# Optimization experiments

Measured on AMD Instinct MI355X. Metric: run time of the kernel, lower is better.

Reference implementation:

```python
import jax, jax.numpy as jnp
from jax import lax
import numpy as np

BATCH = 131072
D_IN = 512
D_OUT = 512
ITERS = 10
THRES = 1e-6


def bjorck_orthonormalize(w, iters=ITERS, thres=THRES):
    """Order-1 Bjorck orthonormalization: W <- 1.5*W - 0.5*W (W^T W).

    Row-orthogonal if out<=in, column-orthogonal otherwise (operate on W^T).
    Early-stops when max|delta| <= thres, matching the module's tolerance.
    """
    transpose = w.shape[0] > w.shape[1]
    if transpose:
        w = w.T

    def cond(state):
        i, _, err = state
        return jnp.logical_and(i < iters, err > thres)

    def body(state):
        i, w, _ = state
        w_new = 1.5 * w - 0.5 * (w @ (w.T @ w))
        err = jnp.max(jnp.abs(w_new - w))
        return i + 1, w_new, err

    _, w, _ = lax.while_loop(
        cond, body, (jnp.array(0, jnp.int32), w, jnp.array(jnp.inf, w.dtype))
    )
    if transpose:
        w = w.T
    return w


def setup_inputs() -> dict:
    key = jax.random.key(0)
    k1, k2 = jax.random.split(key)
    inputs = jax.random.normal(k1, (BATCH, D_IN), dtype=jnp.float32)
    # scaled Gaussian so singular values lie in (0, sqrt(3)) -> Bjorck converges
    weight = jax.random.normal(k2, (D_OUT, D_IN), dtype=jnp.float32) * (0.5 / np.sqrt(D_IN))
    return {"inputs": inputs, "weight": weight}


def reference(inputs, weight):
    # training-mode forward with projection=True, inverse=False:
    # weight.data <- bjorck(weight.data); out = F.linear(inputs, weight)
    w_proj = bjorck_orthonormalize(weight)
    return inputs @ w_proj.T  # [batch, out_features]
```

## Files before the change

### kernel.cpp

```cpp
#include <hip/hip_runtime.h>


using bf16x8 = __attribute__((ext_vector_type(8))) short;
using f32x4  = __attribute__((ext_vector_type(4))) float;
using u16x8  = __attribute__((ext_vector_type(8))) unsigned short;

#define DI 512

__device__ __forceinline__ unsigned short f2bf(float f) {
  unsigned int u = __builtin_bit_cast(unsigned int, f);
  u += 0x7FFFu + ((u >> 16) & 1u);
  return (unsigned short)(u >> 16);
}
__device__ __forceinline__ float bf2f(unsigned short h) {
  unsigned int u = ((unsigned int)h) << 16;
  return __builtin_bit_cast(float, u);
}

__global__ void k_split(const float* __restrict__ W, float* __restrict__ Wm,
                        unsigned short* __restrict__ Wh, unsigned short* __restrict__ Wl,
                        unsigned short* __restrict__ WTh, unsigned short* __restrict__ WTl) {
  int idx = blockIdx.x * blockDim.x + threadIdx.x;
  int m = idx >> 9, i = idx & 511;
  float w = W[idx];
  Wm[idx] = w;
  unsigned short h  = f2bf(w);
  unsigned short lo = f2bf(w - bf2f(h));
  Wh[idx] = h; Wl[idx] = lo;
  WTh[i * DI + m] = h; WTl[i * DI + m] = lo;
}

__global__ __launch_bounds__(256) void k_mm2(
    const unsigned short* __restrict__ Ah, const unsigned short* __restrict__ Al,
    const unsigned short* __restrict__ Bh, const unsigned short* __restrict__ Bl,
    int mode,
    const float* __restrict__ Wm_in, float* __restrict__ Wm_out,
    unsigned short* __restrict__ Oh, unsigned short* __restrict__ Ol,
    unsigned short* __restrict__ OTh, unsigned short* __restrict__ OTl) {
  const int tid = threadIdx.x;
  const int l = tid & 63, lw = tid >> 6;
  const int wid = (blockIdx.x << 2) | lw;
  const int tile = wid >> 1, half = wid & 1;
  const int m0 = (tile >> 5) << 4, n0 = (tile & 31) << 4;
  const int kb = half << 8;
  const int lm = l & 15, lk = l >> 4;
  const int ra = (m0 + lm) * DI + kb + (lk << 3);
  const int rb = (n0 + lm) * DI + kb + (lk << 3);

  __shared__ f32x4 red[2][64];
  const int pr = lw >> 1;

  f32x4 a0{}, a1{}, a2{}, a3{}, a4{}, a5{};
#pragma unroll
  for (int k0 = 0; k0 < 256; k0 += 64) {
    bf16x8 ah0 = *(const bf16x8*)&Ah[ra + k0];
    bf16x8 al0 = *(const bf16x8*)&Al[ra + k0];
    bf16x8 bh0 = *(const bf16x8*)&Bh[rb + k0];
    bf16x8 bl0 = *(const bf16x8*)&Bl[rb + k0];
    bf16x8 ah1 = *(const bf16x8*)&Ah[ra + k0 + 32];
    bf16x8 al1 = *(const bf16x8*)&Al[ra + k0 + 32];
    bf16x8 bh1 = *(const bf16x8*)&Bh[rb + k0 + 32];
    bf16x8 bl1 = *(const bf16x8*)&Bl[rb + k0 + 32];
    a0 = __builtin_amdgcn_mfma_f32_16x16x32_bf16(ah0, bh0, a0, 0, 0, 0);
    a1 = __builtin_amdgcn_mfma_f32_16x16x32_bf16(ah0, bl0, a1, 0, 0, 0);
    a2 = __builtin_amdgcn_mfma_f32_16x16x32_bf16(al0, bh0, a2, 0, 0, 0);
    a3 = __builtin_amdgcn_mfma_f32_16x16x32_bf16(ah1, bh1, a3, 0, 0, 0);
    a4 = __builtin_amdgcn_mfma_f32_16x16x32_bf16(ah1, bl1, a4, 0, 0, 0);
    a5 = __builtin_amdgcn_mfma_f32_16x16x32_bf16(al1, bh1, a5, 0, 0, 0);
  }
  f32x4 acc = (a0 + a1) + (a2 + a3) + (a4 + a5);

  if (half) red[pr][l] = acc;
  __syncthreads();
  if (!half) {
    acc += red[pr][l];
    const int r0 = m0 + (lk << 2);
    const int cn = n0 + lm;
#pragma unroll
    for (int r = 0; r < 4; ++r) {
      const int gm = r0 + r, gn = cn;
      const float v = acc[r];
      if (mode == 0) {
        unsigned short h = f2bf(v);
        Oh[gm * DI + gn] = h;
        Ol[gm * DI + gn] = f2bf(v - bf2f(h));
      } else {
        const float wn = 1.5f * Wm_in[gm * DI + gn] - 0.5f * v;
        Wm_out[gm * DI + gn] = wn;
        unsigned short h = f2bf(wn), lo = f2bf(wn - bf2f(h));
        Oh[gm * DI + gn] = h;   Ol[gm * DI + gn] = lo;
        OTh[gn * DI + gm] = h;  OTl[gn * DI + gm] = lo;
      }
    }
  }
}

#if defined(__has_builtin)
#if __has_builtin(__builtin_amdgcn_global_load_lds)
#define HAVE_GLDS 1
#endif
#endif

#ifdef HAVE_GLDS
__device__ __forceinline__ void gl2lds16(const unsigned short* g, unsigned short* lds) {
  __builtin_amdgcn_global_load_lds(
      (const __attribute__((address_space(1))) void*)g,
      (__attribute__((address_space(3))) void*)lds, 16, 0, 0);
}
#endif

__global__ __launch_bounds__(256, 2) void k_big(
    const float* __restrict__ X, const unsigned short* __restrict__ Wp,
    float* __restrict__ out) {
  __shared__ unsigned short sA[2][2048];
  __shared__ unsigned short sB[2][16384];
  const int tid = threadIdx.x;
  const int w = tid >> 6, l = tid & 63;
  const int lm = l & 15, lk = l >> 4;
  const int ck = lk ^ ((lm >> 1) & 3);
  const int rowbase = blockIdx.x << 6;

  const int arow = tid >> 2, ac = tid & 3;
  const int alds = (arow * 4 + (ac ^ ((arow >> 1) & 3))) * 8;
  const float* xsrc = &X[(rowbase + arow) * DI + ac * 8];

  const int brow_l = l >> 2;
  const int bcs = (l & 3) ^ ((brow_l >> 1) & 3);

  f32x4 acc[4][8] = {};

  auto stage_b = [&](int kk, int bb) {
#pragma unroll
    for (int ph = 0; ph < 8; ++ph) {
      const int rowblk = ph * 64 + w * 16;
      const unsigned short* src = &Wp[(rowblk + brow_l) * DI + (kk << 5) + bcs * 8];
#ifdef HAVE_GLDS
      gl2lds16(src, &sB[bb][rowblk * 32]);
#else
      u16x8 v = *(const u16x8*)src;
      *(u16x8*)&sB[bb][rowblk * 32 + l * 8] = v;
#endif
    }
  };

  f32x4 xv0 = *(const f32x4*)xsrc;
  f32x4 xv1 = *(const f32x4*)(xsrc + 4);
  stage_b(0, 0);
  {
    u16x8 h;
    h[0] = f2bf(xv0[0]); h[1] = f2bf(xv0[1]); h[2] = f2bf(xv0[2]); h[3] = f2bf(xv0[3]);
    h[4] = f2bf(xv1[0]); h[5] = f2bf(xv1[1]); h[6] = f2bf(xv1[2]); h[7] = f2bf(xv1[3]);
    *(u16x8*)&sA[0][alds] = h;
  }
  __syncthreads();

  for (int k = 0; k < 16; ++k) {
    const int buf = k & 1;
    if (k < 15) {
      xv0 = *(const f32x4*)(xsrc + ((k + 1) << 5));
      xv1 = *(const f32x4*)(xsrc + ((k + 1) << 5) + 4);
      stage_b(k + 1, buf ^ 1);
    }
    bf16x8 a[4], b[8];
#pragma unroll
    for (int mf = 0; mf < 4; ++mf)
      a[mf] = *(const bf16x8*)&sA[buf][((mf * 16 + lm) * 4 + ck) * 8];
#pragma unroll
    for (int nf = 0; nf < 8; ++nf)
      b[nf] = *(const bf16x8*)&sB[buf][((w * 128 + nf * 16 + lm) * 4 + ck) * 8];
#pragma unroll
    for (int mf = 0; mf < 4; ++mf)
#pragma unroll
      for (int nf = 0; nf < 8; ++nf)
        acc[mf][nf] = __builtin_amdgcn_mfma_f32_16x16x32_bf16(b[nf], a[mf], acc[mf][nf], 0, 0, 0);
    if (k < 15) {
      u16x8 h;
      h[0] = f2bf(xv0[0]); h[1] = f2bf(xv0[1]); h[2] = f2bf(xv0[2]); h[3] = f2bf(xv0[3]);
      h[4] = f2bf(xv1[0]); h[5] = f2bf(xv1[1]); h[6] = f2bf(xv1[2]); h[7] = f2bf(xv1[3]);
      *(u16x8*)&sA[buf ^ 1][alds] = h;
    }
    __syncthreads();
  }

#pragma unroll
  for (int mf = 0; mf < 4; ++mf) {
    const int gm = rowbase + (mf << 4) + lm;
#pragma unroll
    for (int nf = 0; nf < 8; ++nf) {
      const int gn = (w << 7) + (nf << 4) + (lk << 2);
      *(f32x4*)&out[gm * DI + gn] = acc[mf][nf];
    }
  }
}

extern "C" void kernel_launch(void* const* d_in, const int* in_sizes, int n_in,
                              void* d_out, int out_size, void* d_ws, size_t ws_size,
                              hipStream_t stream) {
  const float* X = (const float*)d_in[0];
  const float* W = (const float*)d_in[1];
  float* out = (float*)d_out;

  char* ws = (char*)d_ws;
  size_t off = 0;
  auto carve = [&](size_t bytes) { void* p = ws + off; off += (bytes + 255) & ~(size_t)255; return p; };

  const size_t F32 = (size_t)DI * DI * 4;
  const size_t BF  = (size_t)DI * DI * 2;

  float* Wm[2];           unsigned short *Wh[2], *Wl[2], *WTh[2], *WTl[2];
  Wm[0]  = (float*)carve(F32);          Wm[1]  = (float*)carve(F32);
  Wh[0]  = (unsigned short*)carve(BF);  Wh[1]  = (unsigned short*)carve(BF);
  Wl[0]  = (unsigned short*)carve(BF);  Wl[1]  = (unsigned short*)carve(BF);
  WTh[0] = (unsigned short*)carve(BF);  WTh[1] = (unsigned short*)carve(BF);
  WTl[0] = (unsigned short*)carve(BF);  WTl[1] = (unsigned short*)carve(BF);
  unsigned short* Gh = (unsigned short*)carve(BF);
  unsigned short* Gl = (unsigned short*)carve(BF);

  k_split<<<1024, 256, 0, stream>>>(W, Wm[0], Wh[0], Wl[0], WTh[0], WTl[0]);

  int cur = 0;
  for (int it = 0; it < 10; ++it) {
    k_mm2<<<512, 256, 0, stream>>>(WTh[cur], WTl[cur], WTh[cur], WTl[cur], 0,
                                   nullptr, nullptr, Gh, Gl, nullptr, nullptr);
    const int nxt = cur ^ 1;
    k_mm2<<<512, 256, 0, stream>>>(Wh[cur], Wl[cur], Gh, Gl, 1,
                                   Wm[cur], Wm[nxt], Wh[nxt], Wl[nxt], WTh[nxt], WTl[nxt]);
    cur = nxt;
  }

  k_big<<<2048, 256, 0, stream>>>(X, Wh[cur], out);
}
```

Measured before the change: 391.2 us.

## Overlap X bf16 conversion with Bjorck iterations using extra blocks

```diff
diff --git a/kernel.cpp b/kernel.cpp
--- a/kernel.cpp
+++ b/kernel.cpp
@@ -6,6 +6,9 @@
 using u16x8  = __attribute__((ext_vector_type(8))) unsigned short;
 
 #define DI 512
+#define MFMA16(a, b, c) __builtin_amdgcn_mfma_f32_16x16x32_bf16(a, b, c, 0, 0, 0)
+#define XTOT 67108864LL
+#define XSLICE 6711296LL
 
 __device__ __forceinline__ unsigned short f2bf(float f) {
   unsigned int u = __builtin_bit_cast(unsigned int, f);
@@ -36,8 +39,25 @@
     int mode,
     const float* __restrict__ Wm_in, float* __restrict__ Wm_out,
     unsigned short* __restrict__ Oh, unsigned short* __restrict__ Ol,
-    unsigned short* __restrict__ OTh, unsigned short* __restrict__ OTl) {
+    unsigned short* __restrict__ OTh, unsigned short* __restrict__ OTl,
+    const float* __restrict__ Xsrc, unsigned short* __restrict__ Xb, int slice) {
   const int tid = threadIdx.x;
+  if (blockIdx.x >= 512) {
+    if (Xb == nullptr) return;
+    long long s0 = (long long)slice * XSLICE;
+    long long send = s0 + XSLICE; if (send > XTOT) send = XTOT;
+    for (long long i = s0 + ((long long)(blockIdx.x - 512) * 256 + tid) * 8;
+         i < send; i += 1024LL * 256 * 8) {
+      f32x4 v0 = *(const f32x4*)&Xsrc[i];
+      f32x4 v1 = *(const f32x4*)&Xsrc[i + 4];
+      u16x8 h;
+      h[0] = f2bf(v0[0]); h[1] = f2bf(v0[1]); h[2] = f2bf(v0[2]); h[3] = f2bf(v0[3]);
+      h[4] = f2bf(v1[0]); h[5] = f2bf(v1[1]); h[6] = f2bf(v1[2]); h[7] = f2bf(v1[3]);
+      *(u16x8*)&Xb[i] = h;
+    }
+    return;
+  }
+
   const int l = tid & 63, lw = tid >> 6;
   const int wid = (blockIdx.x << 2) | lw;
   const int tile = wid >> 1, half = wid & 1;
@@ -61,12 +81,12 @@
     bf16x8 al1 = *(const bf16x8*)&Al[ra + k0 + 32];
     bf16x8 bh1 = *(const bf16x8*)&Bh[rb + k0 + 32];
     bf16x8 bl1 = *(const bf16x8*)&Bl[rb + k0 + 32];
-    a0 = __builtin_amdgcn_mfma_f32_16x16x32_bf16(ah0, bh0, a0, 0, 0, 0);
-    a1 = __builtin_amdgcn_mfma_f32_16x16x32_bf16(ah0, bl0, a1, 0, 0, 0);
-    a2 = __builtin_amdgcn_mfma_f32_16x16x32_bf16(al0, bh0, a2, 0, 0, 0);
-    a3 = __builtin_amdgcn_mfma_f32_16x16x32_bf16(ah1, bh1, a3, 0, 0, 0);
-    a4 = __builtin_amdgcn_mfma_f32_16x16x32_bf16(ah1, bl1, a4, 0, 0, 0);
-    a5 = __builtin_amdgcn_mfma_f32_16x16x32_bf16(al1, bh1, a5, 0, 0, 0);
+    a0 = MFMA16(ah0, bh0, a0);
+    a1 = MFMA16(ah0, bl0, a1);
+    a2 = MFMA16(al0, bh0, a2);
+    a3 = MFMA16(ah1, bh1, a3);
+    a4 = MFMA16(ah1, bl1, a4);
+    a5 = MFMA16(al1, bh1, a5);
   }
   f32x4 acc = (a0 + a1) + (a2 + a3) + (a4 + a5);
 
@@ -109,25 +129,94 @@
 }
 #endif
 
-__global__ __launch_bounds__(256, 2) void k_big(
-    const float* __restrict__ X, const unsigned short* __restrict__ Wp,
+__global__ __launch_bounds__(256, 2) void k_big_bf(
+    const unsigned short* __restrict__ Xb, const unsigned short* __restrict__ Wp,
     float* __restrict__ out) {
-  __shared__ unsigned short sA[2][2048];
+  __shared__ unsigned short sX[2][2048];
   __shared__ unsigned short sB[2][16384];
   const int tid = threadIdx.x;
   const int w = tid >> 6, l = tid & 63;
   const int lm = l & 15, lk = l >> 4;
   const int ck = lk ^ ((lm >> 1) & 3);
   const int rowbase = blockIdx.x << 6;
+  const int lrow = l >> 2;
+  const int lcs = (l & 3) ^ ((lrow >> 1) & 3);
+
+  f32x4 acc[4][8] = {};
+
+  auto stage = [&](int kk, int bb) {
+    const unsigned short* xs =
+        &Xb[(rowbase + (w << 4) + lrow) * DI + (kk << 5) + (lcs << 3)];
+#ifdef HAVE_GLDS
+    gl2lds16(xs, &sX[bb][w << 9]);
+#else
+    *(u16x8*)&sX[bb][(w << 9) + l * 8] = *(const u16x8*)xs;
+#endif
+#pragma unroll
+    for (int ph = 0; ph < 8; ++ph) {
+      const int rowblk = ph * 64 + w * 16;
+      const unsigned short* src =
+          &Wp[(rowblk + lrow) * DI + (kk << 5) + (lcs << 3)];
+#ifdef HAVE_GLDS
+      gl2lds16(src, &sB[bb][rowblk * 32]);
+#else
+      *(u16x8*)&sB[bb][rowblk * 32 + l * 8] = *(const u16x8*)src;
+#endif
+    }
+  };
+
+  stage(0, 0);
+  __syncthreads();
+
+  for (int k = 0; k < 16; ++k) {
+    const int buf = k & 1;
+    if (k < 15) stage(k + 1, buf ^ 1);
+    bf16x8 a[4], b[8];
+#pragma unroll
+    for (int mf = 0; mf < 4; ++mf)
+      a[mf] = *(const bf16x8*)&sX[buf][((mf * 16 + lm) * 4 + ck) * 8];
+#pragma unroll
+    for (int nf = 0; nf < 8; ++nf)
+      b[nf] = *(const bf16x8*)&sB[buf][((w * 128 + nf * 16 + lm) * 4 + ck) * 8];
+#pragma unroll
+    for (int mf = 0; mf < 4; ++mf)
+#pragma unroll
+      for (int nf = 0; nf < 8; ++nf)
+        acc[mf][nf] = MFMA16(b[nf], a[mf], acc[mf][nf]);
+    __syncthreads();
+  }
+
+#pragma unroll
+  for (int mf = 0; mf < 4; ++mf) {
+    const int gm = rowbase + (mf << 4) + lm;
+#pragma unroll
+    for (int nf = 0; nf < 8; ++nf) {
+      const int gn = (w << 7) + (nf << 4) + (lk << 2);
+      *(f32x4*)&out[gm * DI + gn] = acc[mf][nf];
+    }
+  }
+}
+
+__global__ __launch_bounds__(256, 2) void k_big(
+    const float* __restrict__ X, const unsigned short* __restrict__ Wp,
+    float* __restrict__ out) {
+  __shared__ unsigned short sX[2][2048];
+  __shared__ unsigned short sB[2][16384];
+  const int tid = threadIdx.x;
+  const int w = tid >> 6, l = tid & 63;
+  const int lm = l & 15, lk = l >> 4;
+  const int ck = lk ^ ((lm >> 1) & 3);
+  const int rowbase = blockIdx.x << 6;
 
   const int arow = tid >> 2, ac = tid & 3;
   const int alds = (arow * 4 + (ac ^ ((arow >> 1) & 3))) * 8;
-  const float* xsrc = &X[(rowbase + arow) * DI + ac * 8];
+  const float* xsrc = &X[(rowbase + arow) * DI + (ac << 3)];
 
   const int brow_l = l >> 2;
   const int bcs = (l & 3) ^ ((brow_l >> 1) & 3);
 
   f32x4 acc[4][8] = {};
+  f32x4 xv[2];
 
   auto stage_b = [&](int kk, int bb) {
 #pragma unroll
@@ -137,34 +226,40 @@
 #ifdef HAVE_GLDS
       gl2lds16(src, &sB[bb][rowblk * 32]);
 #else
-      u16x8 v = *(const u16x8*)src;
-      *(u16x8*)&sB[bb][rowblk * 32 + l * 8] = v;
+      *(u16x8*)&sB[bb][rowblk * 32 + l * 8] = *(const u16x8*)src;
 #endif
     }
   };
-
-  f32x4 xv0 = *(const f32x4*)xsrc;
-  f32x4 xv1 = *(const f32x4*)(xsrc + 4);
+  auto cvt_write = [&](const f32x4& v0, const f32x4& v1, int bb) {
+    u16x8 h;
+    h[0] = f2bf(v0[0]); h[1] = f2bf(v0[1]); h[2] = f2bf(v0[2]); h[3] = f2bf(v0[3]);
+    h[4] = f2bf(v1[0]); h[5] = f2bf(v1[1]); h[6] = f2bf(v1[2]); h[7] = f2bf(v1[3]);
+    *(u16x8*)&sX[bb][alds] = h;
+  };
+
   stage_b(0, 0);
-  {
-    u16x8 h;
-    h[0] = f2bf(xv0[0]); h[1] = f2bf(xv0[1]); h[2] = f2bf(xv0[2]); h[3] = f2bf(xv0[3]);
-    h[4] = f2bf(xv1[0]); h[5] = f2bf(xv1[1]); h[6] = f2bf(xv1[2]); h[7] = f2bf(xv1[3]);
-    *(u16x8*)&sA[0][alds] = h;
-  }
+  f32x4 t0 = *(const f32x4*)xsrc;
+  f32x4 t1 = *(const f32x4*)(xsrc + 4);
+  xv[0] = *(const f32x4*)(xsrc + 32);
+  xv[1] = *(const f32x4*)(xsrc + 36);
+  cvt_write(t0, t1, 0);
   __syncthreads();
 
   for (int k = 0; k < 16; ++k) {
     const int buf = k & 1;
-    if (k < 15) {
-      xv0 = *(const f32x4*)(xsrc + ((k + 1) << 5));
-      xv1 = *(const f32x4*)(xsrc + ((k + 1) << 5) + 4);
-      stage_b(k + 1, buf ^ 1);
-    }
+    if (k < 15) stage_b(k + 1, buf ^ 1);
+    f32x4 n0, n1;
+    if (k < 14) {
+      n0 = *(const f32x4*)(xsrc + ((k + 2) << 5));
+      n1 = *(const f32x4*)(xsrc + ((k + 2) << 5) + 4);
+    }
+    if (k < 15) cvt_write(xv[0], xv[1], buf ^ 1);
+    if (k < 14) { xv[0] = n0; xv[1] = n1; }
+
     bf16x8 a[4], b[8];
 #pragma unroll
     for (int mf = 0; mf < 4; ++mf)
-      a[mf] = *(const bf16x8*)&sA[buf][((mf * 16 + lm) * 4 + ck) * 8];
+      a[mf] = *(const bf16x8*)&sX[buf][((mf * 16 + lm) * 4 + ck) * 8];
 #pragma unroll
     for (int nf = 0; nf < 8; ++nf)
       b[nf] = *(const bf16x8*)&sB[buf][((w * 128 + nf * 16 + lm) * 4 + ck) * 8];
@@ -172,13 +267,7 @@
     for (int mf = 0; mf < 4; ++mf)
 #pragma unroll
       for (int nf = 0; nf < 8; ++nf)
-        acc[mf][nf] = __builtin_amdgcn_mfma_f32_16x16x32_bf16(b[nf], a[mf], acc[mf][nf], 0, 0, 0);
-    if (k < 15) {
-      u16x8 h;
-      h[0] = f2bf(xv0[0]); h[1] = f2bf(xv0[1]); h[2] = f2bf(xv0[2]); h[3] = f2bf(xv0[3]);
-      h[4] = f2bf(xv1[0]); h[5] = f2bf(xv1[1]); h[6] = f2bf(xv1[2]); h[7] = f2bf(xv1[3]);
-      *(u16x8*)&sA[buf ^ 1][alds] = h;
-    }
+        acc[mf][nf] = MFMA16(b[nf], a[mf], acc[mf][nf]);
     __syncthreads();
   }
 
@@ -216,17 +305,26 @@
   unsigned short* Gh = (unsigned short*)carve(BF);
   unsigned short* Gl = (unsigned short*)carve(BF);
 
+  const size_t XB_BYTES = (size_t)XTOT * 2;
+  unsigned short* Xb = nullptr;
+  if (off + XB_BYTES <= ws_size) Xb = (unsigned short*)carve(XB_BYTES);
+
   k_split<<<1024, 256, 0, stream>>>(W, Wm[0], Wh[0], Wl[0], WTh[0], WTl[0]);
 
   int cur = 0;
   for (int it = 0; it < 10; ++it) {
-    k_mm2<<<512, 256, 0, stream>>>(WTh[cur], WTl[cur], WTh[cur], WTl[cur], 0,
-                                   nullptr, nullptr, Gh, Gl, nullptr, nullptr);
+    k_mm2<<<Xb ? 1536 : 512, 256, 0, stream>>>(
+        WTh[cur], WTl[cur], WTh[cur], WTl[cur], 0,
+        nullptr, nullptr, Gh, Gl, nullptr, nullptr,
+        X, Xb, it);
     const int nxt = cur ^ 1;
-    k_mm2<<<512, 256, 0, stream>>>(Wh[cur], Wl[cur], Gh, Gl, 1,
-                                   Wm[cur], Wm[nxt], Wh[nxt], Wl[nxt], WTh[nxt], WTl[nxt]);
+    k_mm2<<<512, 256, 0, stream>>>(
+        Wh[cur], Wl[cur], Gh, Gl, 1,
+        Wm[cur], Wm[nxt], Wh[nxt], Wl[nxt], WTh[nxt], WTl[nxt],
+        nullptr, nullptr, 0);
     cur = nxt;
   }
 
-  k_big<<<2048, 256, 0, stream>>>(X, Wh[cur], out);
-}
+  if (Xb) k_big_bf<<<2048, 256, 0, stream>>>(Xb, Wh[cur], out);
+  else    k_big<<<2048, 256, 0, stream>>>(X, Wh[cur], out);
+}
```

New measurement: 428.7 us. +9.6%, slower.

## Preload whole X tile into LDS and use 512-thread blocks in big GEMM

Applied to the files above, without the earlier changes.

```diff
diff --git a/kernel.cpp b/kernel.cpp
--- a/kernel.cpp
+++ b/kernel.cpp
@@ -6,6 +6,8 @@
 using u16x8  = __attribute__((ext_vector_type(8))) unsigned short;
 
 #define DI 512
+#define MFMA16(a, b, c) __builtin_amdgcn_mfma_f32_16x16x32_bf16(a, b, c, 0, 0, 0)
+#define SXS 520
 
 __device__ __forceinline__ unsigned short f2bf(float f) {
   unsigned int u = __builtin_bit_cast(unsigned int, f);
@@ -61,12 +63,12 @@
     bf16x8 al1 = *(const bf16x8*)&Al[ra + k0 + 32];
     bf16x8 bh1 = *(const bf16x8*)&Bh[rb + k0 + 32];
     bf16x8 bl1 = *(const bf16x8*)&Bl[rb + k0 + 32];
-    a0 = __builtin_amdgcn_mfma_f32_16x16x32_bf16(ah0, bh0, a0, 0, 0, 0);
-    a1 = __builtin_amdgcn_mfma_f32_16x16x32_bf16(ah0, bl0, a1, 0, 0, 0);
-    a2 = __builtin_amdgcn_mfma_f32_16x16x32_bf16(al0, bh0, a2, 0, 0, 0);
-    a3 = __builtin_amdgcn_mfma_f32_16x16x32_bf16(ah1, bh1, a3, 0, 0, 0);
-    a4 = __builtin_amdgcn_mfma_f32_16x16x32_bf16(ah1, bl1, a4, 0, 0, 0);
-    a5 = __builtin_amdgcn_mfma_f32_16x16x32_bf16(al1, bh1, a5, 0, 0, 0);
+    a0 = MFMA16(ah0, bh0, a0);
+    a1 = MFMA16(ah0, bl0, a1);
+    a2 = MFMA16(al0, bh0, a2);
+    a3 = MFMA16(ah1, bh1, a3);
+    a4 = MFMA16(ah1, bl1, a4);
+    a5 = MFMA16(al1, bh1, a5);
   }
   f32x4 acc = (a0 + a1) + (a2 + a3) + (a4 + a5);
 
@@ -84,12 +86,15 @@
         unsigned short h = f2bf(v);
         Oh[gm * DI + gn] = h;
         Ol[gm * DI + gn] = f2bf(v - bf2f(h));
-      } else {
+      } else if (mode == 1) {
         const float wn = 1.5f * Wm_in[gm * DI + gn] - 0.5f * v;
         Wm_out[gm * DI + gn] = wn;
         unsigned short h = f2bf(wn), lo = f2bf(wn - bf2f(h));
         Oh[gm * DI + gn] = h;   Ol[gm * DI + gn] = lo;
         OTh[gn * DI + gm] = h;  OTl[gn * DI + gm] = lo;
+      } else {
+        const float wn = 1.5f * Wm_in[gm * DI + gn] - 0.5f * v;
+        Oh[gm * DI + gn] = f2bf(wn);
       }
     }
   }
@@ -109,85 +114,76 @@
 }
 #endif
 
-__global__ __launch_bounds__(256, 2) void k_big(
+__global__ __launch_bounds__(512, 1) void k_big(
     const float* __restrict__ X, const unsigned short* __restrict__ Wp,
     float* __restrict__ out) {
-  __shared__ unsigned short sA[2][2048];
-  __shared__ unsigned short sB[2][16384];
+  __shared__ unsigned short sX[64 * SXS];
+  __shared__ unsigned short sB[2][512 * 32];
   const int tid = threadIdx.x;
-  const int w = tid >> 6, l = tid & 63;
+  const int wv = tid >> 6, l = tid & 63;
   const int lm = l & 15, lk = l >> 4;
   const int ck = lk ^ ((lm >> 1) & 3);
+  const int wm = wv >> 2, wn = wv & 3;
   const int rowbase = blockIdx.x << 6;
 
-  const int arow = tid >> 2, ac = tid & 3;
-  const int alds = (arow * 4 + (ac ^ ((arow >> 1) & 3))) * 8;
-  const float* xsrc = &X[(rowbase + arow) * DI + ac * 8];
-
-  const int brow_l = l >> 2;
-  const int bcs = (l & 3) ^ ((brow_l >> 1) & 3);
-
-  f32x4 acc[4][8] = {};
-
+  const int srow = l >> 2;
+  const int scs = (l & 3) ^ ((srow >> 1) & 3);
   auto stage_b = [&](int kk, int bb) {
 #pragma unroll
-    for (int ph = 0; ph < 8; ++ph) {
-      const int rowblk = ph * 64 + w * 16;
-      const unsigned short* src = &Wp[(rowblk + brow_l) * DI + (kk << 5) + bcs * 8];
+    for (int p = 0; p < 4; ++p) {
+      const int rowblk = (wv << 6) + (p << 4);
+      const unsigned short* src = &Wp[(rowblk + srow) * DI + (kk << 5) + (scs << 3)];
 #ifdef HAVE_GLDS
-      gl2lds16(src, &sB[bb][rowblk * 32]);
+      gl2lds16(src, &sB[bb][rowblk << 5]);
 #else
-      u16x8 v = *(const u16x8*)src;
-      *(u16x8*)&sB[bb][rowblk * 32 + l * 8] = v;
+      *(u16x8*)&sB[bb][(rowblk << 5) + l * 8] = *(const u16x8*)src;
 #endif
     }
   };
 
-  f32x4 xv0 = *(const f32x4*)xsrc;
-  f32x4 xv1 = *(const f32x4*)(xsrc + 4);
   stage_b(0, 0);
   {
-    u16x8 h;
-    h[0] = f2bf(xv0[0]); h[1] = f2bf(xv0[1]); h[2] = f2bf(xv0[2]); h[3] = f2bf(xv0[3]);
-    h[4] = f2bf(xv1[0]); h[5] = f2bf(xv1[1]); h[6] = f2bf(xv1[2]); h[7] = f2bf(xv1[3]);
-    *(u16x8*)&sA[0][alds] = h;
+    const int xrow = tid >> 3;
+    const int ci = tid & 7;
+    const float* xp = &X[(rowbase + xrow) * DI];
+#pragma unroll
+    for (int i = 0; i < 8; ++i) {
+      const int c_abs = ci + (i << 3);
+      f32x4 v0 = *(const f32x4*)(xp + c_abs * 8);
+      f32x4 v1 = *(const f32x4*)(xp + c_abs * 8 + 4);
+      u16x8 h;
+      h[0] = f2bf(v0[0]); h[1] = f2bf(v0[1]); h[2] = f2bf(v0[2]); h[3] = f2bf(v0[3]);
+      h[4] = f2bf(v1[0]); h[5] = f2bf(v1[1]); h[6] = f2bf(v1[2]); h[7] = f2bf(v1[3]);
+      *(u16x8*)&sX[xrow * SXS + c_abs * 8] = h;
+    }
   }
   __syncthreads();
 
+  f32x4 acc[2][8] = {};
   for (int k = 0; k < 16; ++k) {
     const int buf = k & 1;
-    if (k < 15) {
-      xv0 = *(const f32x4*)(xsrc + ((k + 1) << 5));
-      xv1 = *(const f32x4*)(xsrc + ((k + 1) << 5) + 4);
-      stage_b(k + 1, buf ^ 1);
-    }
-    bf16x8 a[4], b[8];
-#pragma unroll
-    for (int mf = 0; mf < 4; ++mf)
-      a[mf] = *(const bf16x8*)&sA[buf][((mf * 16 + lm) * 4 + ck) * 8];
+    if (k < 15) stage_b(k + 1, buf ^ 1);
+    bf16x8 a[2], b[8];
+#pragma unroll
+    for (int mf = 0; mf < 2; ++mf)
+      a[mf] = *(const bf16x8*)&sX[((wm << 5) + (mf << 4) + lm) * SXS + (k << 5) + (lk << 3)];
 #pragma unroll
     for (int nf = 0; nf < 8; ++nf)
-      b[nf] = *(const bf16x8*)&sB[buf][((w * 128 + nf * 16 + lm) * 4 + ck) * 8];
-#pragma unroll
-    for (int mf = 0; mf < 4; ++mf)
+      b[nf] = *(const bf16x8*)&sB[buf][(((wn << 7) + (nf << 4) + lm) << 5) + (ck << 3)];
+#pragma unroll
+    for (int mf = 0; mf < 2; ++mf)
 #pragma unroll
       for (int nf = 0; nf < 8; ++nf)
-        acc[mf][nf] = __builtin_amdgcn_mfma_f32_16x16x32_bf16(b[nf], a[mf], acc[mf][nf], 0, 0, 0);
-    if (k < 15) {
-      u16x8 h;
-      h[0] = f2bf(xv0[0]); h[1] = f2bf(xv0[1]); h[2] = f2bf(xv0[2]); h[3] = f2bf(xv0[3]);
-      h[4] = f2bf(xv1[0]); h[5] = f2bf(xv1[1]); h[6] = f2bf(xv1[2]); h[7] = f2bf(xv1[3]);
-      *(u16x8*)&sA[buf ^ 1][alds] = h;
-    }
+        acc[mf][nf] = MFMA16(b[nf], a[mf], acc[mf][nf]);
     __syncthreads();
   }
 
 #pragma unroll
-  for (int mf = 0; mf < 4; ++mf) {
-    const int gm = rowbase + (mf << 4) + lm;
+  for (int mf = 0; mf < 2; ++mf) {
+    const int gm = rowbase + (wm << 5) + (mf << 4) + lm;
 #pragma unroll
     for (int nf = 0; nf < 8; ++nf) {
-      const int gn = (w << 7) + (nf << 4) + (lk << 2);
+      const int gn = (wn << 7) + (nf << 4) + (lk << 2);
       *(f32x4*)&out[gm * DI + gn] = acc[mf][nf];
     }
   }
@@ -223,10 +219,10 @@
     k_mm2<<<512, 256, 0, stream>>>(WTh[cur], WTl[cur], WTh[cur], WTl[cur], 0,
                                    nullptr, nullptr, Gh, Gl, nullptr, nullptr);
     const int nxt = cur ^ 1;
-    k_mm2<<<512, 256, 0, stream>>>(Wh[cur], Wl[cur], Gh, Gl, 1,
+    k_mm2<<<512, 256, 0, stream>>>(Wh[cur], Wl[cur], Gh, Gl, (it == 9) ? 2 : 1,
                                    Wm[cur], Wm[nxt], Wh[nxt], Wl[nxt], WTh[nxt], WTl[nxt]);
     cur = nxt;
   }
 
-  k_big<<<2048, 256, 0, stream>>>(X, Wh[cur], out);
-}
+  k_big<<<2048, 512, 0, stream>>>(X, Wh[cur], out);
+}
```

Result: slower. 429.1 us (+9.7%).
